# Kernel tuning notes

Measured on AMD Instinct MI355X. Metric: run time of the kernel, lower is better.

## Reference

```python
import jax, jax.numpy as jnp
import numpy as np

D_IN = 1024
D_OUT = 1024
N_HEADS = 16
HEAD_DIM = D_OUT // N_HEADS


def setup_inputs() -> dict:
    key = jax.random.key(0)
    ks = jax.random.split(key, 6)
    s = 0.02
    return {
        "x": jax.random.normal(ks[0], (2, 2048, D_IN), dtype=jnp.float32),
        "W_q": jax.random.normal(ks[1], (D_IN, D_OUT), dtype=jnp.float32) * s,
        "W_k": jax.random.normal(ks[2], (D_IN, D_OUT), dtype=jnp.float32) * s,
        "W_v": jax.random.normal(ks[3], (D_IN, D_OUT), dtype=jnp.float32) * s,
        "W_o": jax.random.normal(ks[4], (D_OUT, D_OUT), dtype=jnp.float32) * s,
        "b_o": jax.random.normal(ks[5], (D_OUT,), dtype=jnp.float32) * s,
    }


def reference(x, W_q, W_k, W_v, W_o, b_o):
    b, n, _ = x.shape
    # project and split heads: [b, h, n, d]
    q = (x @ W_q).reshape(b, n, N_HEADS, HEAD_DIM).transpose(0, 2, 1, 3)
    k = (x @ W_k).reshape(b, n, N_HEADS, HEAD_DIM).transpose(0, 2, 1, 3)
    v = (x @ W_v).reshape(b, n, N_HEADS, HEAD_DIM).transpose(0, 2, 1, 3)
    scores = jnp.einsum("bhqd,bhkd->bhqk", q, k)
    # causal mask: positions k > q masked with -inf (applied BEFORE scaling, as in source)
    causal = jnp.tril(jnp.ones((n, n), dtype=bool))
    scores = jnp.where(causal, scores, -jnp.inf)
    scale = HEAD_DIM ** 0.5
    attn = jax.nn.softmax(scores / scale, axis=-1)
    ctx = jnp.einsum("bhqk,bhkd->bhqd", attn, v)
    ctx = ctx.transpose(0, 2, 1, 3).reshape(b, n, D_OUT)
    return ctx @ W_o + b_o
```

## Files before the change

### kernel.cpp

```cpp
#include <hip/hip_runtime.h>
#include <hip/hip_bf16.h>


typedef __bf16 bf16x8 __attribute__((ext_vector_type(8)));
typedef __bf16 bf16x4 __attribute__((ext_vector_type(4)));
typedef float  f32x4  __attribute__((ext_vector_type(4)));

typedef __attribute__((address_space(1))) void gas_void;
typedef __attribute__((address_space(3))) void las_void;

__device__ __forceinline__ void gload_lds16(const void* g, void* l) {
  __builtin_amdgcn_global_load_lds((gas_void*)g, (las_void*)l, 16, 0, 0);
}

#define FULL_DRAIN() asm volatile("s_waitcnt vmcnt(0) lgkmcnt(0)" ::: "memory")
#define SCHED_FENCE() __builtin_amdgcn_sched_barrier(0)

#define QSCALE 0.18033688011112042f

__global__ void cvt_f32_bf16_k(const float* __restrict__ in, __bf16* __restrict__ out, int n4) {
  int i = blockIdx.x * 256 + threadIdx.x;
  if (i >= n4) return;
  float4 v = ((const float4*)in)[i];
  bf16x4 o = { (__bf16)v.x, (__bf16)v.y, (__bf16)v.z, (__bf16)v.w };
  ((bf16x4*)out)[i] = o;
}

__global__ void transpose_w4_k(const float* __restrict__ Wq, const float* __restrict__ Wk,
                               const float* __restrict__ Wv, const float* __restrict__ Wo,
                               __bf16* __restrict__ wtqkv, __bf16* __restrict__ wot) {
  __shared__ float tile[32][33];
  const int z = blockIdx.z;
  const float* in = z == 0 ? Wq : z == 1 ? Wk : z == 2 ? Wv : Wo;
  __bf16* out = z < 3 ? wtqkv + (size_t)z * 1048576 : wot;
  const int bx = blockIdx.x, by = blockIdx.y;
  const int tx = threadIdx.x, ty = threadIdx.y;
#pragma unroll
  for (int i = 0; i < 4; ++i)
    tile[ty + i * 8][tx] = in[(by * 32 + ty + i * 8) * 1024 + bx * 32 + tx];
  __syncthreads();
#pragma unroll
  for (int i = 0; i < 4; ++i)
    out[(size_t)(bx * 32 + ty + i * 8) * 1024 + by * 32 + tx] = (__bf16)tile[tx][ty + i * 8];
}

template<int MODE>
__global__ __launch_bounds__(256) void gemm_bt_k(
    const __bf16* __restrict__ A, const __bf16* __restrict__ Bt,
    __bf16* __restrict__ qo, __bf16* __restrict__ ko, __bf16* __restrict__ vo,
    float* __restrict__ outf, const float* __restrict__ bias)
{
  __shared__ __align__(16) __bf16 As[128 * 32];
  __shared__ __align__(16) __bf16 Bs[128 * 32];

  const int t = threadIdx.x;
  const int l = t & 63;
  const int w = t >> 6;
  const int wr = w >> 1, wc = w & 1;
  const int lr = l & 15;
  const int lk = (l >> 4) * 8;
  const int bm = blockIdx.x, bn = blockIdx.y;

  const __bf16* a0 = A + (size_t)(bm * 128 + (t >> 2)) * 1024 + (t & 3) * 8;
  const __bf16* b0 = Bt + (size_t)(bn * 128 + (t >> 2)) * 1024 + (t & 3) * 8;
  __bf16* asd0 = As + t * 8;
  __bf16* asd1 = As + 2048 + t * 8;
  __bf16* bsd0 = Bs + t * 8;
  __bf16* bsd1 = Bs + 2048 + t * 8;

  f32x4 acc[4][4] = {};

  for (int kt = 0; kt < 32; ++kt) {
    const int k0 = kt * 32;
    gload_lds16(a0 + k0, asd0);
    gload_lds16(a0 + 64 * 1024 + k0, asd1);
    gload_lds16(b0 + k0, bsd0);
    gload_lds16(b0 + 64 * 1024 + k0, bsd1);
    __syncthreads();

    bf16x8 af[4], bfr[4];
#pragma unroll
    for (int m = 0; m < 4; ++m)
      af[m] = *(const bf16x8*)(As + (wr * 64 + m * 16 + lr) * 32 + lk);
#pragma unroll
    for (int n = 0; n < 4; ++n)
      bfr[n] = *(const bf16x8*)(Bs + (wc * 64 + n * 16 + lr) * 32 + lk);
#pragma unroll
    for (int m = 0; m < 4; ++m)
#pragma unroll
      for (int n = 0; n < 4; ++n)
        acc[m][n] = __builtin_amdgcn_mfma_f32_16x16x32_bf16(af[m], bfr[n], acc[m][n], 0, 0, 0);
    __syncthreads();
  }

#pragma unroll
  for (int m = 0; m < 4; ++m) {
    const int rg = bm * 128 + wr * 64 + m * 16 + (l >> 4) * 4;
#pragma unroll
    for (int n = 0; n < 4; ++n) {
      const int cg = bn * 128 + wc * 64 + n * 16 + lr;
      if (MODE == 0) {
        const int proj = cg >> 10, within = cg & 1023;
        const int h = within >> 6, d = within & 63;
#pragma unroll
        for (int r = 0; r < 4; ++r) {
          const int row = rg + r;
          const int b = row >> 11, pos = row & 2047;
          const int bh = b * 16 + h;
          if (proj == 0) {
            qo[((size_t)bh * 2048 + pos) * 64 + d] = (__bf16)(acc[m][n][r] * QSCALE);
          } else if (proj == 1) {
            const int tile = pos >> 6, rr = pos & 63;
            const int off = rr * 128 + ((d * 2) ^ ((rr & 7) << 4));
            *(__bf16*)((char*)ko + ((size_t)bh * 32 + tile) * 8192 + off) = (__bf16)acc[m][n][r];
          } else {
            const int tile = pos >> 6, cc = pos & 63;
            const int off = d * 128 + ((cc * 2) ^ ((d & 7) << 4));
            *(__bf16*)((char*)vo + ((size_t)bh * 32 + tile) * 8192 + off) = (__bf16)acc[m][n][r];
          }
        }
      } else {
#pragma unroll
        for (int r = 0; r < 4; ++r)
          outf[(size_t)(rg + r) * 1024 + cg] = acc[m][n][r] + bias[cg];
      }
    }
  }
}

__device__ __forceinline__ bf16x8 lds_swz(const __bf16* base, int row, int cb) {
  const char* p = (const char*)base + row * 128 + (cb ^ ((row & 7) << 4));
  return *(const bf16x8*)p;
}

__global__ __launch_bounds__(512) void attn_fwd_k(
    const __bf16* __restrict__ Q, const __bf16* __restrict__ K,
    const __bf16* __restrict__ V, __bf16* __restrict__ ctx)
{
  __shared__ __align__(16) char smem[53760];
  __bf16* Kbuf = (__bf16*)smem;
  __bf16* Vbuf = (__bf16*)(smem + 16384);
  __bf16* PsB  = (__bf16*)(smem + 32768);
  float*  LsX  = (float*)(smem + 53248);
  float*  xch  = (float*)smem;

  const int n = blockIdx.x;
  const int bh = (n & 255) >> 3;
  const int pp = n & 7;
  const int qt = (n >> 8) ? pp : 15 - pp;
  const int nkt = 2 * qt + 2;

  const int t = threadIdx.x, l = t & 63, w = t >> 6;
  const int lr = l & 15, lg = l >> 4;
  const int qb = w & 3;
  const int kvh = w >> 2;

  const __bf16* qptr = Q + (size_t)bh * 131072;
  const __bf16* kptr = K + (size_t)bh * 131072;
  const __bf16* vptr = V + (size_t)bh * 131072;
  __bf16* Ps = PsB + w * 1280;

  bf16x8 qf[2][2];
#pragma unroll
  for (int m = 0; m < 2; ++m)
#pragma unroll
    for (int h2 = 0; h2 < 2; ++h2)
      qf[m][h2] = *(const bf16x8*)(qptr + (size_t)(qt * 128 + qb * 32 + m * 16 + lr) * 64 + h2 * 32 + lg * 8);

  f32x4 o[2][4] = {};
  f32x4 lsum[2] = {};

  gload_lds16(kptr + t * 8, Kbuf + t * 8);
  gload_lds16(vptr + t * 8, Vbuf + t * 8);
  FULL_DRAIN();
  __syncthreads();
  SCHED_FENCE();

  for (int kt = 0; kt < nkt; ++kt) {
    const int cur = kt & 1;
    if (kt + 1 < nkt) {
      gload_lds16(kptr + (kt + 1) * 4096 + t * 8, Kbuf + (cur ^ 1) * 4096 + t * 8);
      gload_lds16(vptr + (kt + 1) * 4096 + t * 8, Vbuf + (cur ^ 1) * 4096 + t * 8);
    }
    SCHED_FENCE();
    const __bf16* Kb = Kbuf + cur * 4096;
    const __bf16* Vb = Vbuf + cur * 4096;

    bf16x8 kf[2][2];
#pragma unroll
    for (int ng = 0; ng < 2; ++ng)
#pragma unroll
      for (int h2 = 0; h2 < 2; ++h2)
        kf[ng][h2] = lds_swz(Kb, kvh * 32 + ng * 16 + lr, h2 * 64 + lg * 16);

    f32x4 s[2][2];
#pragma unroll
    for (int m = 0; m < 2; ++m)
#pragma unroll
      for (int ng = 0; ng < 2; ++ng) {
        f32x4 z = {};
        z = __builtin_amdgcn_mfma_f32_16x16x32_bf16(qf[m][0], kf[ng][0], z, 0, 0, 0);
        s[m][ng] = __builtin_amdgcn_mfma_f32_16x16x32_bf16(qf[m][1], kf[ng][1], z, 0, 0, 0);
      }

    if (kt >= 2 * qt) {
#pragma unroll
      for (int m = 0; m < 2; ++m) {
        const int qpos = qt * 128 + qb * 32 + m * 16 + lg * 4;
#pragma unroll
        for (int ng = 0; ng < 2; ++ng) {
          const int kv = kt * 64 + kvh * 32 + ng * 16 + lr;
#pragma unroll
          for (int r = 0; r < 4; ++r)
            if (kv > qpos + r) s[m][ng][r] = -1e30f;
        }
      }
    }

#pragma unroll
    for (int m = 0; m < 2; ++m)
#pragma unroll
      for (int ng = 0; ng < 2; ++ng)
#pragma unroll
        for (int r = 0; r < 4; ++r) {
          const float p = __builtin_amdgcn_exp2f(s[m][ng][r]);
          lsum[m][r] += p;
          Ps[(m * 16 + lg * 4 + r) * 40 + ng * 16 + lr] = (__bf16)p;
        }

    asm volatile("s_waitcnt lgkmcnt(0)" ::: "memory");
    SCHED_FENCE();

    bf16x8 pf[2];
#pragma unroll
    for (int m = 0; m < 2; ++m)
      pf[m] = *(const bf16x8*)(Ps + (m * 16 + lr) * 40 + lg * 8);
    bf16x8 vf[4];
#pragma unroll
    for (int ngd = 0; ngd < 4; ++ngd)
      vf[ngd] = lds_swz(Vb, ngd * 16 + lr, kvh * 64 + lg * 16);
#pragma unroll
    for (int m = 0; m < 2; ++m)
#pragma unroll
      for (int ngd = 0; ngd < 4; ++ngd)
        o[m][ngd] = __builtin_amdgcn_mfma_f32_16x16x32_bf16(pf[m], vf[ngd], o[m][ngd], 0, 0, 0);

    FULL_DRAIN();
    __syncthreads();
    SCHED_FENCE();
  }

#pragma unroll
  for (int m = 0; m < 2; ++m)
#pragma unroll
    for (int r = 0; r < 4; ++r) {
      float v = lsum[m][r];
      v += __shfl_xor(v, 1);
      v += __shfl_xor(v, 2);
      v += __shfl_xor(v, 4);
      v += __shfl_xor(v, 8);
      lsum[m][r] = v;
    }

  if (kvh == 1) {
#pragma unroll
    for (int m = 0; m < 2; ++m)
#pragma unroll
      for (int ngd = 0; ngd < 4; ++ngd)
#pragma unroll
        for (int r = 0; r < 4; ++r)
          xch[qb * 2048 + (m * 16 + lg * 4 + r) * 64 + ngd * 16 + lr] = o[m][ngd][r];
    if (lr == 0) {
#pragma unroll
      for (int m = 0; m < 2; ++m)
#pragma unroll
        for (int r = 0; r < 4; ++r)
          LsX[qb * 32 + m * 16 + lg * 4 + r] = lsum[m][r];
    }
  }
  FULL_DRAIN();
  __syncthreads();
  SCHED_FENCE();

  if (kvh == 0) {
    const int b_ = bh >> 4, h = bh & 15;
#pragma unroll
    for (int m = 0; m < 2; ++m)
#pragma unroll
      for (int r = 0; r < 4; ++r) {
        const float sum = lsum[m][r] + LsX[qb * 32 + m * 16 + lg * 4 + r];
        const float inv = 1.0f / sum;
        const int pos = qt * 128 + qb * 32 + m * 16 + lg * 4 + r;
#pragma unroll
        for (int ngd = 0; ngd < 4; ++ngd) {
          const float val = o[m][ngd][r] +
              xch[qb * 2048 + (m * 16 + lg * 4 + r) * 64 + ngd * 16 + lr];
          ctx[((size_t)(b_ * 2048 + pos)) * 1024 + h * 64 + ngd * 16 + lr] =
              (__bf16)(val * inv);
        }
      }
  }
}

extern "C" void kernel_launch(void* const* d_in, const int* in_sizes, int n_in,
                              void* d_out, int out_size, void* d_ws, size_t ws_size,
                              hipStream_t stream) {
  const float* x  = (const float*)d_in[0];
  const float* Wq = (const float*)d_in[1];
  const float* Wk = (const float*)d_in[2];
  const float* Wv = (const float*)d_in[3];
  const float* Wo = (const float*)d_in[4];
  const float* bo = (const float*)d_in[5];
  float* out = (float*)d_out;

  char* ws = (char*)d_ws;
  __bf16* xb    = (__bf16*)(ws);
  __bf16* wtqkv = (__bf16*)(ws + (8u << 20));
  __bf16* wot   = (__bf16*)(ws + (14u << 20));
  __bf16* qbuf  = (__bf16*)(ws + (16u << 20));
  __bf16* kbuf  = (__bf16*)(ws + (24u << 20));
  __bf16* vbuf  = (__bf16*)(ws + (32u << 20));
  __bf16* ctx   = (__bf16*)(ws + (40u << 20));

  cvt_f32_bf16_k<<<4096, 256, 0, stream>>>(x, xb, 1048576);
  transpose_w4_k<<<dim3(32, 32, 4), dim3(32, 8), 0, stream>>>(Wq, Wk, Wv, Wo, wtqkv, wot);

  gemm_bt_k<0><<<dim3(32, 24), 256, 0, stream>>>(xb, wtqkv, qbuf, kbuf, vbuf, nullptr, nullptr);
  attn_fwd_k<<<512, 512, 0, stream>>>(qbuf, kbuf, vbuf, ctx);
  gemm_bt_k<1><<<dim3(32, 8), 256, 0, stream>>>(ctx, wot, nullptr, nullptr, nullptr, out, bo);
}
```

Measured before the change: 104.7 us.

## Triple-buffer GEMM LDS tiles with async prefetch and XOR swizzle

The projection GEMM now keeps three LDS stages and issues global-to-LDS loads two k-tiles ahead, waiting on vmcnt instead of draining every iteration. This is meant to overlap memory latency with MFMA work. It also XOR-swizzles the 16-byte chunk position per row to reduce LDS bank conflicts on fragment reads. LDS use triples to 48KB per block, which may lower occupancy.

```diff
diff --git a/kernel.cpp b/kernel.cpp
--- a/kernel.cpp
+++ b/kernel.cpp
@@ -44,54 +44,77 @@
     out[(size_t)(bx * 32 + ty + i * 8) * 1024 + by * 32 + tx] = (__bf16)tile[tx][ty + i * 8];
 }
 
+__device__ __forceinline__ bf16x8 lds_swz32(const __bf16* base, int row, int cb) {
+  const char* p = (const char*)base + row * 64 + (cb ^ (((row >> 1) & 3) << 4));
+  return *(const bf16x8*)p;
+}
+
 template<int MODE>
 __global__ __launch_bounds__(256) void gemm_bt_k(
     const __bf16* __restrict__ A, const __bf16* __restrict__ Bt,
     __bf16* __restrict__ qo, __bf16* __restrict__ ko, __bf16* __restrict__ vo,
     float* __restrict__ outf, const float* __restrict__ bias)
 {
-  __shared__ __align__(16) __bf16 As[128 * 32];
-  __shared__ __align__(16) __bf16 Bs[128 * 32];
+  __shared__ __align__(16) __bf16 As[3][4096];
+  __shared__ __align__(16) __bf16 Bs[3][4096];
 
   const int t = threadIdx.x;
   const int l = t & 63;
   const int w = t >> 6;
   const int wr = w >> 1, wc = w & 1;
   const int lr = l & 15;
-  const int lk = (l >> 4) * 8;
+  const int lkb = (l >> 4) * 16;
   const int bm = blockIdx.x, bn = blockIdx.y;
 
-  const __bf16* a0 = A + (size_t)(bm * 128 + (t >> 2)) * 1024 + (t & 3) * 8;
-  const __bf16* b0 = Bt + (size_t)(bn * 128 + (t >> 2)) * 1024 + (t & 3) * 8;
-  __bf16* asd0 = As + t * 8;
-  __bf16* asd1 = As + 2048 + t * 8;
-  __bf16* bsd0 = Bs + t * 8;
-  __bf16* bsd1 = Bs + 2048 + t * 8;
+  const int swz_el = ((t & 3) * 8) ^ (((t >> 3) & 3) << 3);
+  const __bf16* a0 = A + (size_t)(bm * 128 + (t >> 2)) * 1024 + swz_el;
+  const __bf16* b0 = Bt + (size_t)(bn * 128 + (t >> 2)) * 1024 + swz_el;
 
   f32x4 acc[4][4] = {};
 
+#define STAGE(kt_, buf_)                                          \
+  do {                                                            \
+    const int k0_ = (kt_) * 32;                                   \
+    gload_lds16(a0 + k0_, As[buf_] + t * 8);                      \
+    gload_lds16(a0 + 64 * 1024 + k0_, As[buf_] + 2048 + t * 8);   \
+    gload_lds16(b0 + k0_, Bs[buf_] + t * 8);                      \
+    gload_lds16(b0 + 64 * 1024 + k0_, Bs[buf_] + 2048 + t * 8);   \
+  } while (0)
+
+  STAGE(0, 0);
+  STAGE(1, 1);
+  SCHED_FENCE();
+  asm volatile("s_waitcnt vmcnt(4)" ::: "memory");
+  __builtin_amdgcn_s_barrier();
+  SCHED_FENCE();
+
+  int bc = 0, bs = 2;
   for (int kt = 0; kt < 32; ++kt) {
-    const int k0 = kt * 32;
-    gload_lds16(a0 + k0, asd0);
-    gload_lds16(a0 + 64 * 1024 + k0, asd1);
-    gload_lds16(b0 + k0, bsd0);
-    gload_lds16(b0 + 64 * 1024 + k0, bsd1);
-    __syncthreads();
+    if (kt < 30) STAGE(kt + 2, bs);
+    SCHED_FENCE();
 
     bf16x8 af[4], bfr[4];
 #pragma unroll
     for (int m = 0; m < 4; ++m)
-      af[m] = *(const bf16x8*)(As + (wr * 64 + m * 16 + lr) * 32 + lk);
+      af[m] = lds_swz32(As[bc], wr * 64 + m * 16 + lr, lkb);
 #pragma unroll
     for (int n = 0; n < 4; ++n)
-      bfr[n] = *(const bf16x8*)(Bs + (wc * 64 + n * 16 + lr) * 32 + lk);
+      bfr[n] = lds_swz32(Bs[bc], wc * 64 + n * 16 + lr, lkb);
 #pragma unroll
     for (int m = 0; m < 4; ++m)
 #pragma unroll
       for (int n = 0; n < 4; ++n)
         acc[m][n] = __builtin_amdgcn_mfma_f32_16x16x32_bf16(af[m], bfr[n], acc[m][n], 0, 0, 0);
-    __syncthreads();
-  }
+
+    SCHED_FENCE();
+    if (kt < 30) asm volatile("s_waitcnt vmcnt(4)" ::: "memory");
+    else         asm volatile("s_waitcnt vmcnt(0)" ::: "memory");
+    __builtin_amdgcn_s_barrier();
+    SCHED_FENCE();
+    bc = (bc == 2) ? 0 : bc + 1;
+    bs = (bs == 2) ? 0 : bs + 1;
+  }
+#undef STAGE
 
 #pragma unroll
   for (int m = 0; m < 4; ++m) {
```

Result: no change. 106.6 us (+1.8%).
